# Kernel tuning notes

Hardware: AMD Instinct MI355X
Metric: run time of the kernel (lower is better)

## Reference

```python
import jax, jax.numpy as jnp
import numpy as np

B, L, D, H, FF = 32, 577, 512, 8, 2048  # L = sequence_length + 1
DK = D // H
EPS = 1e-6


def setup_inputs() -> dict:
    key = jax.random.key(0)
    ks = jax.random.split(key, 16)
    s = lambda fan_in: 1.0 / np.sqrt(fan_in)
    inp = {
        "x": jax.random.normal(ks[0], (B, L, D), dtype=jnp.float32),
        # whole-sequence LayerNorm params (flattened over L*D)
        "gamma1": jnp.ones((L * D,), jnp.float32),
        "beta1": jnp.zeros((L * D,), jnp.float32),
        "gamma2": jnp.ones((L * D,), jnp.float32),
        "beta2": jnp.zeros((L * D,), jnp.float32),
        # attention projections, stored [in, out] (torch Linear weight transposed)
        "wq": jax.random.uniform(ks[1], (D, D), jnp.float32, -s(D), s(D)),
        "bq": jax.random.uniform(ks[2], (D,), jnp.float32, -s(D), s(D)),
        "wk": jax.random.uniform(ks[3], (D, D), jnp.float32, -s(D), s(D)),
        "bk": jax.random.uniform(ks[4], (D,), jnp.float32, -s(D), s(D)),
        "wv": jax.random.uniform(ks[5], (D, D), jnp.float32, -s(D), s(D)),
        "bv": jax.random.uniform(ks[6], (D,), jnp.float32, -s(D), s(D)),
        "wo": jax.random.uniform(ks[7], (D, D), jnp.float32, -s(D), s(D)),
        "bo": jax.random.uniform(ks[8], (D,), jnp.float32, -s(D), s(D)),
        # FFN 512 -> 2048 -> 512
        "w1": jax.random.uniform(ks[9], (D, FF), jnp.float32, -s(D), s(D)),
        "b1": jax.random.uniform(ks[10], (FF,), jnp.float32, -s(D), s(D)),
        "w2": jax.random.uniform(ks[11], (FF, D), jnp.float32, -s(FF), s(FF)),
        "b2": jax.random.uniform(ks[12], (D,), jnp.float32, -s(FF), s(FF)),
    }
    return inp


def _whole_seq_layernorm(x, gamma, beta):
    # Flattens [B, L, D] -> [B, L*D]; stats over all tokens jointly.
    xf = x.reshape(x.shape[0], -1)
    mean = jnp.mean(xf, axis=-1, keepdims=True)
    std = jnp.std(xf, axis=-1, keepdims=True, ddof=1)  # torch .std() is unbiased
    out = gamma * ((xf - mean) / (std + EPS)) + beta
    return out.reshape(x.shape)


def _mha(x, wq, bq, wk, bk, wv, bv, wo, bo):
    q = (x @ wq + bq).reshape(B, L, H, DK)
    k = (x @ wk + bk).reshape(B, L, H, DK)
    v = (x @ wv + bv).reshape(B, L, H, DK)
    # NOTE: original scales by 1/sqrt(d_model), not 1/sqrt(d_k)
    scores = jnp.einsum("blhd,bmhd->bhlm", q, k) / jnp.sqrt(jnp.float32(D))
    w = jax.nn.softmax(scores, axis=-1)
    o = jnp.einsum("bhlm,bmhd->blhd", w, v).reshape(B, L, D)
    return o @ wo + bo


def reference(x, gamma1, beta1, gamma2, beta2, wq, bq, wk, bk, wv, bv, wo, bo, w1, b1, w2, b2):
    h = _whole_seq_layernorm(x, gamma1, beta1)
    h = _mha(h, wq, bq, wk, bk, wv, bv, wo, bo) + x
    g = _whole_seq_layernorm(h, gamma2, beta2)
    ff = jax.nn.gelu(g @ w1 + b1, approximate=False) @ w2 + b2
    return ff + h
```

## Files before the change

### kernel.cpp

```cpp
#include <hip/hip_runtime.h>
#include <math.h>

typedef unsigned short u16;
typedef __attribute__((ext_vector_type(8))) short short8;
typedef __attribute__((ext_vector_type(4))) float f32x4;
typedef __attribute__((ext_vector_type(16))) float f32x16;

constexpr int NB = 32, NL = 577, ND = 512, NH = 8, NDK = 64, NFF = 2048;
constexpr int NTOK = NB * NL;
constexpr int NLP  = 640;
constexpr int LDN  = NL * ND;
constexpr size_t QKVE = (size_t)NB * NH * NLP * NDK;

__device__ __forceinline__ u16 f2bf(float f) {
  union { float f; unsigned u; } v; v.f = f;
  unsigned r = v.u + 0x7fffu + ((v.u >> 16) & 1u);
  return (u16)(r >> 16);
}
__device__ __forceinline__ float bf2f(u16 h) {
  union { unsigned u; float f; } v; v.u = ((unsigned)h) << 16; return v.f;
}
__device__ __forceinline__ void gload_lds16(const void* g, void* l) {
  __builtin_amdgcn_global_load_lds((const __attribute__((address_space(1))) void*)g,
                                   (__attribute__((address_space(3))) void*)l, 16, 0, 0);
}
__device__ __forceinline__ int xcd_swz(int lin, int nwg) {
  const int xcd = lin & 7, o = lin >> 3;
  const int q = nwg >> 3, r = nwg & 7;
  return (xcd < r ? xcd * (q + 1) : r * (q + 1) + (xcd - r) * q) + o;
}
__device__ __forceinline__ unsigned cvt_pk_bf16(float a, float b) {
  unsigned r;
  asm("v_cvt_pk_bf16_f32 %0, %1, %2" : "=v"(r) : "v"(a), "v"(b));
  return r;
}
__device__ __forceinline__ float exp2_f(float x) {
  float r;
  asm("v_exp_f32 %0, %1" : "=v"(r) : "v"(x));
  return r;
}
__device__ __forceinline__ short8 mk8(unsigned a, unsigned b, unsigned c, unsigned d) {
  union { unsigned u[4]; short8 v; } f;
  f.u[0] = a; f.u[1] = b; f.u[2] = c; f.u[3] = d;
  return f.v;
}
__device__ __forceinline__ f32x16 mfma32(short8 a, short8 b, f32x16 c) {
  return __builtin_amdgcn_mfma_f32_32x32x16_bf16(a, b, c, 0, 0, 0);
}
__device__ __forceinline__ f32x4 mfma16(short8 a, short8 b, f32x4 c) {
  return __builtin_amdgcn_mfma_f32_16x16x32_bf16(a, b, c, 0, 0, 0);
}

__global__ void pad_zero(u16* __restrict__ qb, u16* __restrict__ kb, u16* __restrict__ vt,
                         float* __restrict__ stats,
                         const float* __restrict__ bq, const float* __restrict__ bk,
                         const float* __restrict__ bv, float* __restrict__ cbias) {
  const int i = blockIdx.x * 256 + threadIdx.x;
  if (i < 128) stats[i] = 0.f;
  if (i < 1536) cbias[i] = i < 512 ? bq[i] : (i < 1024 ? bk[i - 512] : bv[i - 1024]);
  const int NPQ = 256 * 63 * 64;
  if (i < NPQ) {
    const int bh = i / (63 * 64), rem = i - bh * (63 * 64);
    const int r = rem >> 6, d = rem & 63;
    const size_t o = ((size_t)bh * NLP + 577 + r) * NDK + d;
    qb[o] = 0; kb[o] = 0;
    const int d2 = rem / 63, kv = rem - d2 * 63;
    vt[((size_t)bh * NDK + d2) * NLP + 577 + kv] = 0;
  }
}

__global__ void ln_stats(const float* __restrict__ x, float* __restrict__ stats) {
  const int b = blockIdx.x, s = blockIdx.y;
  const int per4 = LDN / 8 / 4;
  const float4* xb = (const float4*)(x + (size_t)b * LDN + (size_t)s * (LDN / 8));
  float sum = 0.f, ss = 0.f;
  for (int i = threadIdx.x; i < per4; i += blockDim.x) {
    float4 v = xb[i];
    sum += v.x + v.y + v.z + v.w;
    ss  += v.x * v.x + v.y * v.y + v.z * v.z + v.w * v.w;
  }
#pragma unroll
  for (int o = 32; o; o >>= 1) { sum += __shfl_down(sum, o); ss += __shfl_down(ss, o); }
  __shared__ float s0[4], s1[4];
  const int lane = threadIdx.x & 63, w = threadIdx.x >> 6;
  if (lane == 0) { s0[w] = sum; s1[w] = ss; }
  __syncthreads();
  if (threadIdx.x == 0) {
    atomicAdd(&stats[b * 2 + 0], s0[0] + s0[1] + s0[2] + s0[3]);
    atomicAdd(&stats[b * 2 + 1], s1[0] + s1[1] + s1[2] + s1[3]);
  }
}

__global__ void ln_apply(const float* __restrict__ x, const float* __restrict__ stats,
                         const float* __restrict__ gamma, const float* __restrict__ beta,
                         u16* __restrict__ out) {
  const int nv = LDN / 4;
  const size_t total = (size_t)NB * nv;
  for (size_t i = (size_t)blockIdx.x * blockDim.x + threadIdx.x; i < total;
       i += (size_t)gridDim.x * blockDim.x) {
    const int b = (int)(i / nv);
    const int j = (int)(i - (size_t)b * nv);
    const float sum = stats[b * 2], ssum = stats[b * 2 + 1];
    const float mean = sum / (float)LDN;
    const float var = (ssum - (float)LDN * mean * mean) / (float)(LDN - 1);
    const float inv = 1.0f / (sqrtf(var) + 1e-6f);
    const float4 xv = ((const float4*)x)[i];
    const float4 gv = ((const float4*)gamma)[j];
    const float4 bv = ((const float4*)beta)[j];
    ushort4 o;
    o.x = f2bf(gv.x * ((xv.x - mean) * inv) + bv.x);
    o.y = f2bf(gv.y * ((xv.y - mean) * inv) + bv.y);
    o.z = f2bf(gv.z * ((xv.z - mean) * inv) + bv.z);
    o.w = f2bf(gv.w * ((xv.w - mean) * inv) + bv.w);
    ((ushort4*)out)[i] = o;
  }
}

__global__ void ln_apply_b(const u16* __restrict__ x, const float* __restrict__ stats,
                           const float* __restrict__ gamma, const float* __restrict__ beta,
                           u16* __restrict__ out) {
  const int nv = LDN / 4;
  const size_t total = (size_t)NB * nv;
  for (size_t i = (size_t)blockIdx.x * blockDim.x + threadIdx.x; i < total;
       i += (size_t)gridDim.x * blockDim.x) {
    const int b = (int)(i / nv);
    const int j = (int)(i - (size_t)b * nv);
    const float sum = stats[b * 2], ssum = stats[b * 2 + 1];
    const float mean = sum / (float)LDN;
    const float var = (ssum - (float)LDN * mean * mean) / (float)(LDN - 1);
    const float inv = 1.0f / (sqrtf(var) + 1e-6f);
    const ushort4 xv = ((const ushort4*)x)[i];
    const float4 gv = ((const float4*)gamma)[j];
    const float4 bv = ((const float4*)beta)[j];
    ushort4 o;
    o.x = f2bf(gv.x * ((bf2f(xv.x) - mean) * inv) + bv.x);
    o.y = f2bf(gv.y * ((bf2f(xv.y) - mean) * inv) + bv.y);
    o.z = f2bf(gv.z * ((bf2f(xv.z) - mean) * inv) + bv.z);
    o.w = f2bf(gv.w * ((bf2f(xv.w) - mean) * inv) + bv.w);
    ((ushort4*)out)[i] = o;
  }
}

__global__ void transpose_bf16(const float* __restrict__ w, u16* __restrict__ wt,
                               int K, int N) {
  const size_t total = (size_t)K * N;
  for (size_t i = (size_t)blockIdx.x * blockDim.x + threadIdx.x; i < total;
       i += (size_t)gridDim.x * blockDim.x) {
    const int k = (int)(i / N), n = (int)(i - (size_t)k * N);
    wt[(size_t)n * K + k] = f2bf(w[i]);
  }
}
__global__ void transpose_qkv(const float* __restrict__ wq, const float* __restrict__ wk,
                              const float* __restrict__ wv, u16* __restrict__ wt) {
  const size_t total = (size_t)1536 * 512;
  for (size_t i = (size_t)blockIdx.x * blockDim.x + threadIdx.x; i < total;
       i += (size_t)gridDim.x * blockDim.x) {
    const int n = (int)(i >> 9), k = (int)(i & 511);
    const int s = n >> 9, c = n & 511;
    const float* src = s == 0 ? wq : (s == 1 ? wk : wv);
    wt[i] = f2bf(src[(size_t)k * 512 + c]);
  }
}

template <int EPI>
__global__ __launch_bounds__(256, 4) void gemm_bt(
    const u16* __restrict__ A, const u16* __restrict__ Bt,
    int M, int N, int K, int lda, int ldb,
    const float* __restrict__ bias,
    void* __restrict__ outp, float oscale) {
  __shared__ __align__(16) u16 lA[128 * 64];
  __shared__ __align__(16) u16 lB[128 * 64];
  int lin = blockIdx.x + blockIdx.y * gridDim.x;
  lin = xcd_swz(lin, gridDim.x * gridDim.y);
  const int bx = lin / gridDim.y, by = lin - (lin / gridDim.y) * gridDim.y;
  const int m0 = bx * 128, n0 = by * 128;
  const int tid = threadIdx.x, lane = tid & 63, wid = tid >> 6;
  const int l16 = lane & 15, l4 = lane >> 4;
  const int wm = wid >> 1, wn = wid & 1;

  f32x4 acc[4][4] = {};

  for (int k0 = 0; k0 < K; k0 += 64) {
#pragma unroll
    for (int j = 0; j < 4; j++) {
      const int cb = j * 256 + wid * 64;
      const int c = cb + lane;
      const int row = c >> 3, g = c & 7;
      const int scol = k0 + ((g ^ (row & 7)) << 3);
      gload_lds16(A + (size_t)(m0 + row) * lda + scol, &lA[cb * 8]);
      gload_lds16(Bt + (size_t)(n0 + row) * ldb + scol, &lB[cb * 8]);
    }
    __syncthreads();
#pragma unroll
    for (int ks = 0; ks < 2; ks++) {
      short8 af[4], bfr[4];
#pragma unroll
      for (int mi = 0; mi < 4; mi++) {
        const int rl = wm * 64 + mi * 16 + l16;
        af[mi] = *(const short8*)&lA[rl * 64 + (((ks * 4 + l4) ^ (rl & 7)) << 3)];
      }
#pragma unroll
      for (int ni = 0; ni < 4; ni++) {
        const int rl = wn * 64 + ni * 16 + l16;
        bfr[ni] = *(const short8*)&lB[rl * 64 + (((ks * 4 + l4) ^ (rl & 7)) << 3)];
      }
#pragma unroll
      for (int mi = 0; mi < 4; mi++)
#pragma unroll
        for (int ni = 0; ni < 4; ni++)
          acc[mi][ni] = mfma16(af[mi], bfr[ni], acc[mi][ni]);
    }
    __syncthreads();
  }

#pragma unroll
  for (int mi = 0; mi < 4; mi++) {
#pragma unroll
    for (int r = 0; r < 4; r++) {
      const int row = m0 + wm * 64 + mi * 16 + l4 * 4 + r;
      if (row >= M) continue;
      int rb = 0, rl = 0;
      if (EPI == 0) { rb = row / NL; rl = row - rb * NL; }
#pragma unroll
      for (int ni = 0; ni < 4; ni++) {
        const int col = n0 + wn * 64 + ni * 16 + l16;
        if (col >= N) continue;
        const float v = acc[mi][ni][r];
        if (EPI == 0) {
          const int kind = col >> 9, c = col & 511, h = c >> 6, d = c & 63;
          const float val = v + bias[col];
          u16* base = (u16*)outp;
          if (kind == 0)
            base[(((size_t)rb * NH + h) * NLP + rl) * NDK + d] = f2bf(val * oscale);
          else if (kind == 1)
            (base + QKVE)[(((size_t)rb * NH + h) * NLP + rl) * NDK + d] = f2bf(val);
          else
            (base + 2 * QKVE)[(((size_t)rb * NH + h) * NDK + d) * NLP + rl] = f2bf(val);
        } else {
          const float t = v + bias[col];
          const float u = 0.7978845608028654f * t * (1.0f + 0.044715f * t * t);
          const float e = __expf(-2.0f * fabsf(u));
          float th = (1.0f - e) * __builtin_amdgcn_rcpf(1.0f + e);
          th = u < 0.f ? -th : th;
          ((u16*)outp)[(size_t)row * N + col] = f2bf(0.5f * t * (1.0f + th));
        }
      }
    }
  }
}

template <int EPI>
__global__ __launch_bounds__(128, 4) void gemm_sm(
    const u16* __restrict__ A, const u16* __restrict__ Bt,
    int M, int N, int K, int lda, int ldb,
    const float* __restrict__ bias,
    const void* __restrict__ res, int ldr,
    void* __restrict__ outp, float* __restrict__ stats) {
  __shared__ __align__(16) u16 lA[64 * 64];
  __shared__ __align__(16) u16 lB[128 * 64];
  int lin = blockIdx.x + blockIdx.y * gridDim.x;
  lin = xcd_swz(lin, gridDim.x * gridDim.y);
  const int bx = lin / gridDim.y, by = lin - (lin / gridDim.y) * gridDim.y;
  const int m0 = bx * 64, n0 = by * 128;
  const int tid = threadIdx.x, lane = tid & 63, wid = tid >> 6;
  const int l16 = lane & 15, l4 = lane >> 4;

  f32x4 acc[4][4] = {};

  for (int k0 = 0; k0 < K; k0 += 64) {
#pragma unroll
    for (int j = 0; j < 4; j++) {
      const int cb = j * 128 + wid * 64;
      const int c = cb + lane;
      const int row = c >> 3, g = c & 7;
      gload_lds16(A + (size_t)(m0 + row) * lda + k0 + ((g ^ (row & 7)) << 3), &lA[cb * 8]);
    }
#pragma unroll
    for (int j = 0; j < 8; j++) {
      const int cb = j * 128 + wid * 64;
      const int c = cb + lane;
      const int row = c >> 3, g = c & 7;
      gload_lds16(Bt + (size_t)(n0 + row) * ldb + k0 + ((g ^ (row & 7)) << 3), &lB[cb * 8]);
    }
    __syncthreads();
#pragma unroll
    for (int ks = 0; ks < 2; ks++) {
      short8 af[4], bfr[4];
#pragma unroll
      for (int mi = 0; mi < 4; mi++) {
        const int rl = mi * 16 + l16;
        af[mi] = *(const short8*)&lA[rl * 64 + (((ks * 4 + l4) ^ (rl & 7)) << 3)];
      }
#pragma unroll
      for (int ni = 0; ni < 4; ni++) {
        const int rl = wid * 64 + ni * 16 + l16;
        bfr[ni] = *(const short8*)&lB[rl * 64 + (((ks * 4 + l4) ^ (rl & 7)) << 3)];
      }
#pragma unroll
      for (int mi = 0; mi < 4; mi++)
#pragma unroll
        for (int ni = 0; ni < 4; ni++)
          acc[mi][ni] = mfma16(af[mi], bfr[ni], acc[mi][ni]);
    }
    __syncthreads();
  }

  float sm0 = 0.f, sm1 = 0.f, sq0 = 0.f, sq1 = 0.f;
#pragma unroll
  for (int mi = 0; mi < 4; mi++) {
#pragma unroll
    for (int r = 0; r < 4; r++) {
      const int row = m0 + mi * 16 + l4 * 4 + r;
      if (row >= M) continue;
      int which = 0;
      if (EPI == 6) which = (row >= (m0 / NL + 1) * NL) ? 1 : 0;
#pragma unroll
      for (int ni = 0; ni < 4; ni++) {
        const int col = n0 + wid * 64 + ni * 16 + l16;
        const float v = acc[mi][ni][r];
        if (EPI == 6) {
          const float hv = v + bias[col] + ((const float*)res)[(size_t)row * ldr + col];
          ((u16*)outp)[(size_t)row * N + col] = f2bf(hv);
          if (which) { sm1 += hv; sq1 += hv * hv; }
          else       { sm0 += hv; sq0 += hv * hv; }
        } else {
          ((float*)outp)[(size_t)row * N + col] =
              v + bias[col] + bf2f(((const u16*)res)[(size_t)row * ldr + col]);
        }
      }
    }
  }
  if (EPI == 6) {
#pragma unroll
    for (int o = 32; o; o >>= 1) {
      sm0 += __shfl_down(sm0, o); sq0 += __shfl_down(sq0, o);
      sm1 += __shfl_down(sm1, o); sq1 += __shfl_down(sq1, o);
    }
    if (lane == 0) {
      const int b0 = m0 / NL;
      atomicAdd(&stats[b0 * 2 + 0], sm0);
      atomicAdd(&stats[b0 * 2 + 1], sq0);
      if (b0 + 1 < NB) {
        atomicAdd(&stats[(b0 + 1) * 2 + 0], sm1);
        atomicAdd(&stats[(b0 + 1) * 2 + 1], sq1);
      }
    }
  }
}

__global__ __launch_bounds__(64, 2) void attn_fused(
    const u16* __restrict__ qb, const u16* __restrict__ kb,
    const u16* __restrict__ vt, u16* __restrict__ aog) {
  const int lane = threadIdx.x & 63;
  const int l32 = lane & 31, hi = lane >> 5;
  int lin = blockIdx.x + blockIdx.y * gridDim.x;
  lin = xcd_swz(lin, gridDim.x * gridDim.y);
  const int qt = lin % 10, bh = lin / 10;
  const int q0 = qt * 64;
  const u16* QpA = qb + (size_t)bh * NLP * NDK + (size_t)(q0 + l32) * NDK + hi * 8;
  const u16* Kp = kb + (size_t)bh * NLP * NDK + (size_t)l32 * NDK + hi * 8;
  const u16* Vp = vt + (size_t)bh * NDK * NLP + (size_t)l32 * NLP + hi * 8;

  short8 qfA[4], qfB[4];
#pragma unroll
  for (int kc = 0; kc < 4; kc++) {
    qfA[kc] = *(const short8*)(QpA + kc * 16);
    qfB[kc] = *(const short8*)(QpA + (size_t)32 * NDK + kc * 16);
  }

  f32x16 oA0 = {}, oA1 = {}, oB0 = {}, oB1 = {};
  float mA = -3e38f, lA = 0.f, mB = -3e38f, lB = 0.f;

  for (int kv0 = 0; kv0 < NLP; kv0 += 64) {
    short8 ka[4], kh[4];
#pragma unroll
    for (int kc = 0; kc < 4; kc++) {
      ka[kc] = *(const short8*)(Kp + (size_t)kv0 * NDK + kc * 16);
      kh[kc] = *(const short8*)(Kp + (size_t)(kv0 + 32) * NDK + kc * 16);
    }
    f32x16 sA0 = {}, sA1 = {}, sB0 = {}, sB1 = {};
    __builtin_amdgcn_s_setprio(1);
#pragma unroll
    for (int kc = 0; kc < 4; kc++) {
      sA0 = mfma32(ka[kc], qfA[kc], sA0);
      sA1 = mfma32(kh[kc], qfA[kc], sA1);
      sB0 = mfma32(ka[kc], qfB[kc], sB0);
      sB1 = mfma32(kh[kc], qfB[kc], sB1);
    }
    __builtin_amdgcn_s_setprio(0);
    short8 vf0[4], vf1[4];
#pragma unroll
    for (int ks = 0; ks < 4; ks++) {
      vf0[ks] = *(const short8*)(Vp + (size_t)(kv0 + ks * 16));
      vf1[ks] = *(const short8*)(Vp + (size_t)32 * NLP + (kv0 + ks * 16));
    }
    if (kv0 + 64 > NL) {
#pragma unroll
      for (int r = 0; r < 16; r++) {
        const int kvb = kv0 + (r & 3) + 8 * (r >> 2) + 4 * hi;
        const bool v0 = kvb < NL, v1 = kvb + 32 < NL;
        sA0[r] = v0 ? sA0[r] : -1e30f;
        sA1[r] = v1 ? sA1[r] : -1e30f;
        sB0[r] = v0 ? sB0[r] : -1e30f;
        sB1[r] = v1 ? sB1[r] : -1e30f;
      }
    }
#pragma unroll
    for (int half = 0; half < 2; half++) {
      f32x16& s0 = half ? sB0 : sA0;
      f32x16& s1 = half ? sB1 : sA1;
      f32x16& o0 = half ? oB0 : oA0;
      f32x16& o1 = half ? oB1 : oA1;
      float& m = half ? mB : mA;
      float& l = half ? lB : lA;
      float t4[8];
#pragma unroll
      for (int i = 0; i < 8; i++)
        t4[i] = fmaxf(fmaxf(s0[2 * i], s0[2 * i + 1]), fmaxf(s1[2 * i], s1[2 * i + 1]));
      float t = fmaxf(fmaxf(fmaxf(t4[0], t4[1]), fmaxf(t4[2], t4[3])),
                      fmaxf(fmaxf(t4[4], t4[5]), fmaxf(t4[6], t4[7])));
      t = fmaxf(t, __shfl_xor(t, 32));
      if (!__all(t - m <= 8.0f)) {
        const float mn = fmaxf(m, t);
        const float sc = exp2_f(m - mn);
        m = mn;
        l *= sc;
#pragma unroll
        for (int r = 0; r < 16; r++) { o0[r] *= sc; o1[r] *= sc; }
      }
      float rs = 0.f;
#pragma unroll
      for (int r = 0; r < 16; r++) { s0[r] = exp2_f(s0[r] - m); rs += s0[r]; }
#pragma unroll
      for (int r = 0; r < 16; r++) { s1[r] = exp2_f(s1[r] - m); rs += s1[r]; }
      l += rs + __shfl_xor(rs, 32);

      unsigned w0[8], w1[8], p0[8], p1[8];
#pragma unroll
      for (int i = 0; i < 8; i++) {
        w0[i] = cvt_pk_bf16(s0[2 * i], s0[2 * i + 1]);
        w1[i] = cvt_pk_bf16(s1[2 * i], s1[2 * i + 1]);
      }
#pragma unroll
      for (int i = 0; i < 8; i++) {
        p0[i] = (unsigned)__shfl_xor((int)w0[i], 32);
        p1[i] = (unsigned)__shfl_xor((int)w1[i], 32);
      }
      short8 pa[4];
      pa[0] = mk8(hi ? p0[2] : w0[0], hi ? p0[3] : w0[1], hi ? w0[2] : p0[0], hi ? w0[3] : p0[1]);
      pa[1] = mk8(hi ? p0[6] : w0[4], hi ? p0[7] : w0[5], hi ? w0[6] : p0[4], hi ? w0[7] : p0[5]);
      pa[2] = mk8(hi ? p1[2] : w1[0], hi ? p1[3] : w1[1], hi ? w1[2] : p1[0], hi ? w1[3] : p1[1]);
      pa[3] = mk8(hi ? p1[6] : w1[4], hi ? p1[7] : w1[5], hi ? w1[6] : p1[4], hi ? w1[7] : p1[5]);
      __builtin_amdgcn_s_setprio(1);
#pragma unroll
      for (int ks = 0; ks < 4; ks++) {
        o0 = mfma32(vf0[ks], pa[ks], o0);
        o1 = mfma32(vf1[ks], pa[ks], o1);
      }
      __builtin_amdgcn_s_setprio(0);
    }
  }

  const int b = bh >> 3, h = bh & 7;
#pragma unroll
  for (int half = 0; half < 2; half++) {
    const int qg = q0 + half * 32 + l32;
    if (qg >= NL) continue;
    const f32x16& o0 = half ? oB0 : oA0;
    const f32x16& o1 = half ? oB1 : oA1;
    const float inv = 1.0f / (half ? lB : lA);
    u16* orow = aog + ((size_t)b * NL + qg) * ND + h * NDK;
#pragma unroll
    for (int r = 0; r < 16; r += 2) {
      const int d = (r & 3) + 4 * hi + 8 * (r >> 2);
      *(unsigned*)(orow + d) = cvt_pk_bf16(o0[r] * inv, o0[r + 1] * inv);
      *(unsigned*)(orow + 32 + d) = cvt_pk_bf16(o1[r] * inv, o1[r + 1] * inv);
    }
  }
}

extern "C" void kernel_launch(void* const* d_in, const int* in_sizes, int n_in,
                              void* d_out, int out_size, void* d_ws, size_t ws_size,
                              hipStream_t stream) {
  const float* x      = (const float*)d_in[0];
  const float* gamma1 = (const float*)d_in[1];
  const float* beta1  = (const float*)d_in[2];
  const float* gamma2 = (const float*)d_in[3];
  const float* beta2  = (const float*)d_in[4];
  const float* wq = (const float*)d_in[5];
  const float* bq = (const float*)d_in[6];
  const float* wk = (const float*)d_in[7];
  const float* bk = (const float*)d_in[8];
  const float* wv = (const float*)d_in[9];
  const float* bv = (const float*)d_in[10];
  const float* wo = (const float*)d_in[11];
  const float* bo = (const float*)d_in[12];
  const float* w1 = (const float*)d_in[13];
  const float* b1 = (const float*)d_in[14];
  const float* w2 = (const float*)d_in[15];
  const float* b2 = (const float*)d_in[16];
  float* out = (float*)d_out;

  char* ws = (char*)d_ws;
  size_t off = 0;
  auto take = [&](size_t bytes) { size_t o = off; off += (bytes + 255) & ~(size_t)255; return o; };
  const size_t SLK = 2u << 20;

  float* stats = (float*)(ws + take(512));
  float* stats1 = stats;
  float* stats2 = stats + 64;
  float* cbias = (float*)(ws + take(1536 * 4));
  u16* wqkvT = (u16*)(ws + take((size_t)1536 * 512 * 2));
  u16* woT = (u16*)(ws + take((size_t)512 * 512 * 2));
  u16* w1T = (u16*)(ws + take((size_t)512 * 2048 * 2));
  u16* w2T = (u16*)(ws + take((size_t)2048 * 512 * 2));
  u16* hbuf = (u16*)(ws + take((size_t)NTOK * ND * 2 + SLK));
  u16* qb = (u16*)(ws + take(3 * QKVE * 2 + SLK));
  u16* kb = qb + QKVE;
  u16* vt = kb + QKVE;
  u16* aog = (u16*)(ws + take((size_t)NTOK * ND * 2 + SLK));
  size_t r7 = take((size_t)NTOK * NFF * 2 + SLK);
  u16* xn   = (u16*)(ws + r7);
  u16* ubuf = (u16*)(ws + r7);

  pad_zero<<<(256 * 63 * 64 + 255) / 256, 256, 0, stream>>>(qb, kb, vt, stats, bq, bk, bv, cbias);

  transpose_qkv<<<1536, 256, 0, stream>>>(wq, wk, wv, wqkvT);
  transpose_bf16<<<512, 256, 0, stream>>>(wo, woT, 512, 512);
  transpose_bf16<<<2048, 256, 0, stream>>>(w1, w1T, 512, 2048);
  transpose_bf16<<<2048, 256, 0, stream>>>(w2, w2T, 2048, 512);

  ln_stats<<<dim3(NB, 8), 256, 0, stream>>>(x, stats1);
  ln_apply<<<2048, 256, 0, stream>>>(x, stats1, gamma1, beta1, xn);

  constexpr float QSCALE = 0.04419417382415922f * 1.4426950408889634f;
  gemm_bt<0><<<dim3(145, 12), 256, 0, stream>>>(xn, wqkvT, NTOK, 1536, ND, ND, ND,
                                                cbias, qb, QSCALE);

  attn_fused<<<dim3(10, NB * NH), 64, 0, stream>>>(qb, kb, vt, aog);

  gemm_sm<6><<<dim3(289, 4), 128, 0, stream>>>(aog, woT, NTOK, ND, ND, ND, ND,
                                               bo, x, ND, hbuf, stats2);

  ln_apply_b<<<2048, 256, 0, stream>>>(hbuf, stats2, gamma2, beta2, aog);

  gemm_bt<5><<<dim3(145, 16), 256, 0, stream>>>(aog, w1T, NTOK, NFF, ND, ND, ND,
                                                b1, ubuf, 1.0f);
  gemm_sm<4><<<dim3(289, 4), 128, 0, stream>>>(ubuf, w2T, NTOK, ND, NFF, NFF, NFF,
                                               b2, hbuf, ND, out, nullptr);
}
```

Before: 429.3 us.

## Replace LDS-staged output-projection GEMM with register-direct 128x128 tile kernel

Adds a gemm_reg kernel that loads A and B fragments straight from global memory into registers, with no LDS staging or barriers. It uses 128x128 tiles across four waves and fuses the bias plus residual add and the per-batch LayerNorm sum and sum-of-squares atomics. The output-projection GEMM now uses this kernel in place of gemm_sm<6>, and the EPI==6 path is removed from gemm_sm. The trade is less synchronization and LDS traffic against relying on L1/L2 for reuse between waves, with less latency hiding. The last row tile reads A rows past M.

```diff
diff --git a/kernel.cpp b/kernel.cpp
--- a/kernel.cpp
+++ b/kernel.cpp
@@ -305,45 +305,89 @@
     __syncthreads();
   }
 
-  float sm0 = 0.f, sm1 = 0.f, sq0 = 0.f, sq1 = 0.f;
 #pragma unroll
   for (int mi = 0; mi < 4; mi++) {
 #pragma unroll
     for (int r = 0; r < 4; r++) {
       const int row = m0 + mi * 16 + l4 * 4 + r;
       if (row >= M) continue;
-      int which = 0;
-      if (EPI == 6) which = (row >= (m0 / NL + 1) * NL) ? 1 : 0;
 #pragma unroll
       for (int ni = 0; ni < 4; ni++) {
         const int col = n0 + wid * 64 + ni * 16 + l16;
         const float v = acc[mi][ni][r];
-        if (EPI == 6) {
-          const float hv = v + bias[col] + ((const float*)res)[(size_t)row * ldr + col];
-          ((u16*)outp)[(size_t)row * N + col] = f2bf(hv);
-          if (which) { sm1 += hv; sq1 += hv * hv; }
-          else       { sm0 += hv; sq0 += hv * hv; }
-        } else {
-          ((float*)outp)[(size_t)row * N + col] =
-              v + bias[col] + bf2f(((const u16*)res)[(size_t)row * ldr + col]);
-        }
-      }
-    }
-  }
-  if (EPI == 6) {
-#pragma unroll
-    for (int o = 32; o; o >>= 1) {
-      sm0 += __shfl_down(sm0, o); sq0 += __shfl_down(sq0, o);
-      sm1 += __shfl_down(sm1, o); sq1 += __shfl_down(sq1, o);
-    }
-    if (lane == 0) {
-      const int b0 = m0 / NL;
-      atomicAdd(&stats[b0 * 2 + 0], sm0);
-      atomicAdd(&stats[b0 * 2 + 1], sq0);
-      if (b0 + 1 < NB) {
-        atomicAdd(&stats[(b0 + 1) * 2 + 0], sm1);
-        atomicAdd(&stats[(b0 + 1) * 2 + 1], sq1);
-      }
+        ((float*)outp)[(size_t)row * N + col] =
+            v + bias[col] + bf2f(((const u16*)res)[(size_t)row * ldr + col]);
+      }
+    }
+  }
+}
+
+template <int EPI, int KT>
+__global__ __launch_bounds__(256, 3) void gemm_reg(
+    const u16* __restrict__ A, const u16* __restrict__ Bt,
+    int M, int N, int lda, int ldb,
+    const float* __restrict__ bias,
+    const void* __restrict__ res, int ldr,
+    void* __restrict__ outp, float* __restrict__ stats) {
+  int lin = blockIdx.x + blockIdx.y * gridDim.x;
+  lin = xcd_swz(lin, gridDim.x * gridDim.y);
+  const int bx = lin / gridDim.y, by = lin - (lin / gridDim.y) * gridDim.y;
+  const int m0 = bx * 128, n0 = by * 128;
+  const int lane = threadIdx.x & 63, wid = threadIdx.x >> 6;
+  const int l16 = lane & 15, l4 = lane >> 4;
+  const int wm = wid >> 1, wn = wid & 1;
+
+  const u16* Ab = A + (size_t)(m0 + wm * 64 + l16) * lda + l4 * 8;
+  const u16* Bb = Bt + (size_t)(n0 + wn * 64 + l16) * ldb + l4 * 8;
+
+  f32x4 acc[4][4] = {};
+#pragma unroll 2
+  for (int k0 = 0; k0 < KT; k0 += 32) {
+    short8 af[4], bfr[4];
+#pragma unroll
+    for (int mi = 0; mi < 4; mi++)
+      af[mi] = *(const short8*)(Ab + (size_t)mi * 16 * lda + k0);
+#pragma unroll
+    for (int ni = 0; ni < 4; ni++)
+      bfr[ni] = *(const short8*)(Bb + (size_t)ni * 16 * ldb + k0);
+#pragma unroll
+    for (int mi = 0; mi < 4; mi++)
+#pragma unroll
+      for (int ni = 0; ni < 4; ni++)
+        acc[mi][ni] = mfma16(af[mi], bfr[ni], acc[mi][ni]);
+  }
+
+  float sm0 = 0.f, sm1 = 0.f, sq0 = 0.f, sq1 = 0.f;
+#pragma unroll
+  for (int mi = 0; mi < 4; mi++) {
+#pragma unroll
+    for (int r = 0; r < 4; r++) {
+      const int row = m0 + wm * 64 + mi * 16 + l4 * 4 + r;
+      if (row >= M) continue;
+      const int which = (row >= (m0 / NL + 1) * NL) ? 1 : 0;
+#pragma unroll
+      for (int ni = 0; ni < 4; ni++) {
+        const int col = n0 + wn * 64 + ni * 16 + l16;
+        const float v = acc[mi][ni][r];
+        const float hv = v + bias[col] + ((const float*)res)[(size_t)row * ldr + col];
+        ((u16*)outp)[(size_t)row * N + col] = f2bf(hv);
+        if (which) { sm1 += hv; sq1 += hv * hv; }
+        else       { sm0 += hv; sq0 += hv * hv; }
+      }
+    }
+  }
+#pragma unroll
+  for (int o = 32; o; o >>= 1) {
+    sm0 += __shfl_down(sm0, o); sq0 += __shfl_down(sq0, o);
+    sm1 += __shfl_down(sm1, o); sq1 += __shfl_down(sq1, o);
+  }
+  if (lane == 0) {
+    const int b0 = m0 / NL;
+    atomicAdd(&stats[b0 * 2 + 0], sm0);
+    atomicAdd(&stats[b0 * 2 + 1], sq0);
+    if (b0 + 1 < NB) {
+      atomicAdd(&stats[(b0 + 1) * 2 + 0], sm1);
+      atomicAdd(&stats[(b0 + 1) * 2 + 1], sq1);
     }
   }
 }
@@ -539,8 +583,8 @@
 
   attn_fused<<<dim3(10, NB * NH), 64, 0, stream>>>(qb, kb, vt, aog);
 
-  gemm_sm<6><<<dim3(289, 4), 128, 0, stream>>>(aog, woT, NTOK, ND, ND, ND, ND,
-                                               bo, x, ND, hbuf, stats2);
+  gemm_reg<6, 512><<<dim3(145, 4), 256, 0, stream>>>(aog, woT, NTOK, ND, ND, ND,
+                                                     bo, x, ND, hbuf, stats2);
 
   ln_apply_b<<<2048, 256, 0, stream>>>(hbuf, stats2, gamma2, beta2, aog);
 
```

New measurement: 453.0 us. 1.06x slower.
